# Kernel tuning notes

Measured on AMD Instinct MI355X. Metric: run time of the kernel, lower is better.

## Reference

```python
import jax, jax.numpy as jnp
import numpy as np

B, S, Dm = 2, 4096, 1024
H, HD = 8, 128            # num_heads, head_dim
WIN, STRIDE = 512, 256    # window_size, window_size // 2
NGT = 64                  # num_global_tokens


def setup_inputs() -> dict:
    key = jax.random.key(0)
    ks = jax.random.split(key, 6)
    sc = lambda k, shape: jax.random.normal(k, shape, jnp.float32) * 0.02
    return {
        "hidden_states": jax.random.normal(ks[0], (B, S, Dm), jnp.float32),
        "global_memory": jax.random.normal(ks[1], (1, H, NGT, HD), jnp.float32),
        "conv_w": sc(ks[2], (Dm, Dm, 4)),   # (out_ch, in_ch, kernel)
        "conv_b": jnp.zeros((Dm,), jnp.float32),
        "mix_w": sc(ks[3], (2 * Dm, Dm)),
        "mix_b": jnp.zeros((Dm,), jnp.float32),
        "out_w": sc(ks[4], (Dm, Dm)),
        "out_b": jnp.zeros((Dm,), jnp.float32),
    }


def _sliding_window(x):
    nw = (S - WIN) // STRIDE + 1
    idx = np.arange(nw)[:, None] * STRIDE + np.arange(WIN)[None, :]
    w = x[:, idx, :].reshape(B, nw, WIN, H, HD)
    att = jnp.einsum('bnqhd,bnkhd->bnhqk', w, w) / np.sqrt(HD).astype(np.float32)
    att = jax.nn.softmax(att, axis=-1)
    o = jnp.einsum('bnhqk,bnkhd->bnqhd', att, w).reshape(B, nw, WIN, Dm)
    # triangular-weighted overlap-add (every window has full length here)
    tri = jnp.linspace(0.5, 1.5, WIN, dtype=x.dtype)
    contrib = (o * tri[None, None, :, None]).reshape(B, nw * WIN, Dm)
    ids = jnp.asarray(idx.reshape(-1))
    num = jax.ops.segment_sum(jnp.moveaxis(contrib, 1, 0), ids, num_segments=S)  # (S,B,Dm)
    den = jax.ops.segment_sum(jnp.tile(tri, nw), ids, num_segments=S)            # (S,)
    return jnp.moveaxis(num, 0, 1) / jnp.maximum(den, 1e-6)[None, :, None]


def _compressed_global(x, gmem, cw, cb):
    # Conv1d(k=4, stride=4) == blockwise contraction over non-overlapping groups of 4
    comp = jnp.einsum('btkd,odk->bto', x.reshape(B, S // 4, 4, Dm), cw) + cb
    comp = comp[:, :NGT].reshape(B, NGT, H, HD).transpose(0, 2, 1, 3)  # (B,H,NGT,HD)
    kv = jnp.concatenate([comp, jnp.broadcast_to(gmem, (B, H, NGT, HD))], axis=2)
    q = x.reshape(B, S, H, HD).transpose(0, 2, 1, 3)                    # (B,H,S,HD)
    att = jax.nn.softmax(jnp.einsum('bhsd,bhtd->bhst', q, kv) / np.sqrt(HD).astype(np.float32), axis=-1)
    out = jnp.einsum('bhst,bhtd->bhsd', att, kv)
    return out.transpose(0, 2, 1, 3).reshape(B, S, Dm)


def _broadcast(x):
    # exponential diffusion: O(log n) roll steps (12 for S=4096)
    result = jnp.zeros_like(x)
    cur = x
    stride = 1
    while stride < S:
        cur = cur + 0.5 * (jnp.roll(cur, stride, axis=1) + jnp.roll(cur, -stride, axis=1))
        result = result + cur
        stride *= 2
    return result / np.float32(np.log2(S) + 1.0)


def reference(hidden_states, global_memory, conv_w, conv_b, mix_w, mix_b, out_w, out_b):
    local = _sliding_window(hidden_states)
    glob = _compressed_global(hidden_states, global_memory, conv_w, conv_b)
    bc = _broadcast(hidden_states)
    gate = jax.nn.sigmoid(jnp.concatenate([local, glob], axis=-1) @ mix_w + mix_b)
    mixed = gate * local + (1.0 - gate) * glob + bc
    return mixed @ out_w + out_b
```

## Files before the change

### kernel.cpp

```cpp
#include <hip/hip_runtime.h>
#include <cstdint>

#define B_   2
#define S_   4096
#define DM   1024
#define NH   8
#define HDIM 128
#define NWIN 15

typedef __attribute__((ext_vector_type(8))) short s8v;
typedef __attribute__((ext_vector_type(4))) float f4v;

__device__ __forceinline__ float f_lo(unsigned int u){
  union { unsigned int i; float f; } v; v.i = u << 16; return v.f;
}
__device__ __forceinline__ float f_hi(unsigned int u){
  union { unsigned int i; float f; } v; v.i = u & 0xffff0000u; return v.f;
}
__device__ __forceinline__ unsigned short f2bf(float f){
  unsigned int x = __float_as_uint(f);
  x += 0x7fffu + ((x >> 16) & 1u);
  return (unsigned short)(x >> 16);
}
__device__ __forceinline__ unsigned int pack2(float a, float b){
  return (unsigned int)f2bf(a) | ((unsigned int)f2bf(b) << 16);
}

__global__ __launch_bounds__(256) void k_cvtbf(const float* __restrict__ src,
                                               unsigned short* __restrict__ dst){
  size_t i = ((size_t)blockIdx.x*256 + threadIdx.x)*8;
  float4 a = *(const float4*)(src + i);
  float4 b = *(const float4*)(src + i + 4);
  uint4 r; r.x = pack2(a.x,a.y); r.y = pack2(a.z,a.w);
  r.z = pack2(b.x,b.y); r.w = pack2(b.z,b.w);
  *(uint4*)(dst + i) = r;
}

__global__ __launch_bounds__(256) void k_xposef(const float* __restrict__ x,
                                                float* __restrict__ xT){
  __shared__ float Ls[64][68];
  const int bid = blockIdx.x;
  const int b = bid>>10, r = bid&1023, st = r>>4, dt = r&15;
  const int s0 = st*64, d0 = dt*64;
  const int tid = threadIdx.x;
#pragma unroll
  for(int p=0;p<4;p++){
    int rr = p*16 + (tid>>4), c4 = (tid&15)*4;
    *(float4*)&Ls[rr][c4] = *(const float4*)(x + ((size_t)(b*S_)+s0+rr)*DM + d0 + c4);
  }
  __syncthreads();
#pragma unroll
  for(int p=0;p<4;p++){
    int dr = p*16 + (tid>>4), c4 = (tid&15)*4;
    float4 v = { Ls[c4+0][dr], Ls[c4+1][dr], Ls[c4+2][dr], Ls[c4+3][dr] };
    *(float4*)(xT + ((size_t)(b*DM)+d0+dr)*S_ + s0 + c4) = v;
  }
}

__global__ __launch_bounds__(256) void k_diffuseT(const float* __restrict__ xT,
                                                  unsigned short* __restrict__ bcT){
  __shared__ float bufA[2][4096];
  __shared__ float bufB[2][4096];
  const int b  = blockIdx.x >> 9;
  const int d0 = (blockIdx.x & 511) * 2;
  const int tid = threadIdx.x;
  float cur[32], res[32];
#pragma unroll
  for(int k=0;k<32;k++){
    int e = tid + (k<<8); int ch = e>>12; int s = e&4095;
    float v = xT[((size_t)(b*DM)+d0+ch)*S_ + s];
    cur[k] = v; res[k] = 0.f; bufA[ch][s] = v;
  }
  __syncthreads();
#pragma unroll 1
  for(int st=0; st<12; st++){
    const int stride = 1<<st;
    float (*src)[4096] = (st&1) ? bufB : bufA;
    float (*dst)[4096] = (st&1) ? bufA : bufB;
#pragma unroll
    for(int k=0;k<32;k++){
      int e = tid + (k<<8); int ch=e>>12; int s=e&4095;
      float c = cur[k] + 0.5f*(src[ch][(s-stride)&4095] + src[ch][(s+stride)&4095]);
      dst[ch][s] = c; cur[k] = c; res[k] += c;
    }
    __syncthreads();
  }
#pragma unroll
  for(int k=0;k<32;k++){
    int e = tid + (k<<8); int ch=e>>12; int s=e&4095;
    bcT[((size_t)(b*DM)+d0+ch)*S_ + s] = f2bf(res[k]*(1.0f/13.0f));
  }
}

__global__ __launch_bounds__(256) void k_bcxpose(const unsigned short* __restrict__ bcT,
                                                 unsigned short* __restrict__ bc){
  __shared__ unsigned short Ls[64*72];
  const int bid = blockIdx.x;
  const int b = bid>>10, r = bid&1023, st = r>>4, dt = r&15;
  const int s0 = st*64, d0 = dt*64;
  const int tid = threadIdx.x;
#pragma unroll
  for(int t=0;t<2;t++){
    int cl = tid + t*256; int dr = cl>>3, c = cl&7;
    *(uint4*)&Ls[dr*72 + c*8] = *(const uint4*)(bcT + ((size_t)(b*DM)+d0+dr)*S_ + s0 + c*8);
  }
  __syncthreads();
#pragma unroll
  for(int t=0;t<2;t++){
    int cl = tid + t*256; int sr = cl>>3, c = cl&7;
    unsigned short tmp[8];
#pragma unroll
    for(int j=0;j<8;j++) tmp[j] = Ls[(c*8+j)*72 + sr];
    *(uint4*)(bc + ((size_t)(b*S_)+s0+sr)*DM + d0 + c*8) = *(const uint4*)tmp;
  }
}

__global__ __launch_bounds__(256) void k_xstage(const float* __restrict__ x,
                                                unsigned short* __restrict__ Asta){
  __shared__ float xs[4][1024];
  const int m = blockIdx.x;
  const int b = m>>6, t = m&63;
  const int tid = threadIdx.x;
  const float* xp = x + (size_t)(b*S_ + 4*t)*DM;
  for(int i=tid; i<4096; i+=256) xs[i>>10][i&1023] = xp[i];
  __syncthreads();
  float v[16];
#pragma unroll
  for(int e=0; e<16; e++) v[e] = xs[e&3][tid*4 + (e>>2)];
  uint4 r0, r1;
  r0.x = pack2(v[0],v[1]);  r0.y = pack2(v[2],v[3]);
  r0.z = pack2(v[4],v[5]);  r0.w = pack2(v[6],v[7]);
  r1.x = pack2(v[8],v[9]);  r1.y = pack2(v[10],v[11]);
  r1.z = pack2(v[12],v[13]); r1.w = pack2(v[14],v[15]);
  unsigned short* op = Asta + (size_t)m*4096 + tid*16;
  *(uint4*)op = r0;
  *(uint4*)(op+8) = r1;
}

__global__ __launch_bounds__(256) void k_gemmconv(const unsigned short* __restrict__ A,
                                                  const unsigned short* __restrict__ Bw,
                                                  float* __restrict__ part){
  __shared__ __align__(16) unsigned short As[128*64];
  __shared__ __align__(16) unsigned short Bs[128*64];
  const int nt = blockIdx.x, kt = blockIdx.y;
  const int n0 = nt<<7;
  const int tid = threadIdx.x, wid = tid>>6, lane = tid&63, quad = lane>>4, tl = lane&15;
  const int mq = (wid&1)*64, nq = (wid>>1)*64;
  f4v acc[4][4];
#pragma unroll
  for(int i=0;i<4;i++)
#pragma unroll
    for(int j=0;j<4;j++) acc[i][j] = (f4v)(0.f);

  for(int kc=kt*1024; kc<kt*1024+1024; kc+=64){
    __syncthreads();
#pragma unroll
    for(int t=0; t<4; t++){
      int cl = tid + t*256, m = cl>>3, c = cl&7;
      uint4 v = *(const uint4*)(A + (size_t)m*4096 + kc + c*8);
      *(uint4*)&As[m*64 + ((c ^ (m&7))<<3)] = v;
      uint4 w = *(const uint4*)(Bw + (size_t)(n0+m)*4096 + kc + c*8);
      *(uint4*)&Bs[m*64 + ((c ^ (m&7))<<3)] = w;
    }
    __syncthreads();
#pragma unroll
    for(int ks=0; ks<2; ks++){
      s8v af[4], bf[4];
#pragma unroll
      for(int i=0;i<4;i++){
        int ml = mq + i*16 + tl;
        af[i] = *(const s8v*)&As[ml*64 + (((ks*4+quad) ^ (ml&7))<<3)];
      }
#pragma unroll
      for(int j=0;j<4;j++){
        int nl = nq + j*16 + tl;
        bf[j] = *(const s8v*)&Bs[nl*64 + (((ks*4+quad) ^ (nl&7))<<3)];
      }
#pragma unroll
      for(int i=0;i<4;i++)
#pragma unroll
        for(int j=0;j<4;j++)
          acc[i][j] = __builtin_amdgcn_mfma_f32_16x16x32_bf16(af[i], bf[j], acc[i][j], 0, 0, 0);
    }
  }
  float* pp = part + (size_t)kt*131072;
#pragma unroll
  for(int i=0;i<4;i++)
#pragma unroll
    for(int r=0;r<4;r++){
      int m = mq + i*16 + quad*4 + r;
#pragma unroll
      for(int j=0;j<4;j++){
        int n = n0 + nq + j*16 + tl;
        pp[m*1024 + n] = acc[i][j][r];
      }
    }
}

__global__ __launch_bounds__(256) void k_convred(const float* __restrict__ part,
                                                 const float* __restrict__ cb,
                                                 unsigned short* __restrict__ kv){
  int i = blockIdx.x*256 + threadIdx.x;
  int m = i>>10, o = i&1023;
  float v = part[i] + part[131072+i] + part[262144+i] + part[393216+i] + cb[o];
  int b = m>>6, t = m&63, h = o>>7, hd = o&127;
  kv[((size_t)(b*NH + h)*128 + t)*HDIM + hd] = f2bf(v);
}

__global__ __launch_bounds__(256) void k_gmem(const float* __restrict__ g,
                                              unsigned short* __restrict__ kv){
  int i = blockIdx.x*256 + threadIdx.x;
  int hd = i & 127, gt = (i>>7)&63, h = (i>>13)&7, b = i>>16;
  kv[((size_t)(b*NH + h)*128 + 64 + gt)*HDIM + hd] = f2bf(g[((size_t)(h*64 + gt))*HDIM + hd]);
}

template<int MODE>
__global__ __launch_bounds__(256) void k_attn(const unsigned short* __restrict__ xb,
                                              const unsigned short* __restrict__ kvb,
                                              unsigned short* __restrict__ outb){
  __shared__ __align__(16) unsigned short sh[26624];
  constexpr int KSo = 0;
  constexpr int VTo = 8192;
  constexpr int PSo = 17408;

  const int b = blockIdx.y;
  int h, n, qt, nkt;
  if(MODE==0){ int r = blockIdx.x; n = r>>5; h = (r>>2)&7; qt = r&3; nkt = 8; }
  else       { int r = blockIdx.x; h = r>>5; qt = r&31; n = 0; nkt = 2; }

  const int tid  = threadIdx.x;
  const int wid  = tid>>6, lane = tid&63, quad = lane>>4, tl = lane&15;
  const int sQ   = (MODE==0) ? (n*256 + qt*128) : (qt*128);

  s8v qf[2][4];
#pragma unroll
  for(int qi=0; qi<2; qi++){
    int qr = sQ + wid*32 + qi*16 + tl;
    const unsigned short* qp = xb + ((size_t)(b*S_) + qr)*DM + h*HDIM;
#pragma unroll
    for(int ks=0; ks<4; ks++)
      qf[qi][ks] = *(const s8v*)(qp + ks*32 + quad*8);
  }

  f4v oacc[8][2];
#pragma unroll
  for(int ht=0; ht<8; ht++){ oacc[ht][0] = (f4v)(0.f); oacc[ht][1] = (f4v)(0.f); }
  float m_[2] = {-1e30f, -1e30f}, l_[2] = {0.f, 0.f};

  for(int kt=0; kt<nkt; kt++){
    __syncthreads();
    const unsigned short* kp = (MODE==0)
        ? xb + ((size_t)(b*S_) + n*256 + kt*64)*DM + h*HDIM
        : kvb + ((size_t)(b*NH+h)*128 + kt*64)*HDIM;
    const int kstride = (MODE==0) ? DM : HDIM;
#pragma unroll
    for(int t=0; t<4; t++){
      int cl = tid + t*256, m = cl>>4, c = cl&15;
      uint4 v = *(const uint4*)(kp + (size_t)m*kstride + c*8);
      *(uint4*)&sh[KSo + m*128 + ((c ^ (m&7))<<3)] = v;
    }
    {
      int hd = tid&127, th = tid>>7;
#pragma unroll
      for(int tt=0; tt<8; tt++){
        int t0 = th*32 + tt*4;
        ushort4 u = { kp[(size_t)(t0+0)*kstride + hd], kp[(size_t)(t0+1)*kstride + hd],
                      kp[(size_t)(t0+2)*kstride + hd], kp[(size_t)(t0+3)*kstride + hd] };
        *(ushort4*)&sh[VTo + hd*72 + t0] = u;
      }
    }
    __syncthreads();

    f4v st[4][2];
#pragma unroll
    for(int tt=0; tt<4; tt++){
      st[tt][0] = (f4v)(0.f); st[tt][1] = (f4v)(0.f);
      int row = tt*16 + tl;
#pragma unroll
      for(int ks=0; ks<4; ks++){
        s8v af = *(const s8v*)&sh[KSo + row*128 + (((ks*4+quad) ^ (row&7))<<3)];
        st[tt][0] = __builtin_amdgcn_mfma_f32_16x16x32_bf16(af, qf[0][ks], st[tt][0], 0, 0, 0);
        st[tt][1] = __builtin_amdgcn_mfma_f32_16x16x32_bf16(af, qf[1][ks], st[tt][1], 0, 0, 0);
      }
    }

    const float SC = 0.08838834764831845f;
#pragma unroll
    for(int qi=0; qi<2; qi++){
      float mx = -1e30f;
#pragma unroll
      for(int tt=0; tt<4; tt++)
#pragma unroll
        for(int r=0; r<4; r++){
          float v = st[tt][qi][r]*SC;
          st[tt][qi][r] = v;
          mx = fmaxf(mx, v);
        }
      mx = fmaxf(mx, __shfl_xor(mx, 16));
      mx = fmaxf(mx, __shfl_xor(mx, 32));
      float nm = fmaxf(m_[qi], mx);
      float al = __expf(m_[qi] - nm);
      float ps = 0.f;
#pragma unroll
      for(int tt=0; tt<4; tt++)
#pragma unroll
        for(int r=0; r<4; r++){
          float p = __expf(st[tt][qi][r] - nm);
          st[tt][qi][r] = p; ps += p;
        }
      ps += __shfl_xor(ps, 16);
      ps += __shfl_xor(ps, 32);
      l_[qi] = l_[qi]*al + ps; m_[qi] = nm;
#pragma unroll
      for(int ht=0; ht<8; ht++) oacc[ht][qi] *= al;
      int ql = wid*32 + qi*16 + tl;
#pragma unroll
      for(int tt=0; tt<4; tt++){
        ushort4 u = { f2bf(st[tt][qi][0]), f2bf(st[tt][qi][1]),
                      f2bf(st[tt][qi][2]), f2bf(st[tt][qi][3]) };
        *(ushort4*)&sh[PSo + ql*72 + tt*16 + quad*4] = u;
      }
    }

#pragma unroll
    for(int kk=0; kk<2; kk++){
      s8v pb0 = *(const s8v*)&sh[PSo + (wid*32 + 0*16 + tl)*72 + kk*32 + quad*8];
      s8v pb1 = *(const s8v*)&sh[PSo + (wid*32 + 1*16 + tl)*72 + kk*32 + quad*8];
#pragma unroll
      for(int ht=0; ht<8; ht++){
        s8v vf = *(const s8v*)&sh[VTo + (ht*16 + tl)*72 + kk*32 + quad*8];
        oacc[ht][0] = __builtin_amdgcn_mfma_f32_16x16x32_bf16(vf, pb0, oacc[ht][0], 0, 0, 0);
        oacc[ht][1] = __builtin_amdgcn_mfma_f32_16x16x32_bf16(vf, pb1, oacc[ht][1], 0, 0, 0);
      }
    }
  }

#pragma unroll
  for(int qi=0; qi<2; qi++){
    float inv = 1.0f/l_[qi];
#pragma unroll
    for(int ht=0; ht<8; ht++) oacc[ht][qi] *= inv;
  }
  __syncthreads();
#pragma unroll
  for(int qi=0; qi<2; qi++){
    int ql = wid*32 + qi*16 + tl;
#pragma unroll
    for(int ht=0; ht<8; ht++){
      ushort4 u = { f2bf(oacc[ht][qi][0]), f2bf(oacc[ht][qi][1]),
                    f2bf(oacc[ht][qi][2]), f2bf(oacc[ht][qi][3]) };
      *(ushort4*)&sh[ql*136 + ht*16 + quad*4] = u;
    }
  }
  __syncthreads();
  {
    int ql = tid>>1, half = tid&1;
    size_t row = (MODE==0) ? (size_t)((b*NWIN + n)*512 + qt*128 + ql)
                           : (size_t)(b*S_ + qt*128 + ql);
    unsigned short* op = outb + row*DM + h*HDIM + half*64;
#pragma unroll
    for(int c=0; c<8; c++){
      uint4 v = *(const uint4*)&sh[ql*136 + half*64 + c*8];
      *(uint4*)(op + c*8) = v;
    }
  }
}

__global__ __launch_bounds__(256) void k_combine(const unsigned short* __restrict__ wso,
                                                 unsigned short* __restrict__ loc){
  const int bid = blockIdx.x;
  const int b = bid >> 12, s = bid & 4095;
  const int tid = threadIdx.x;
  const int nhi = s >> 8, sl = s & 255;
  const int c0 = tid*4;
  float n0=0.f, n1=0.f, n2=0.f, n3=0.f, den=0.f;
  if(nhi <= 14){
    float tr = 0.5f + (float)sl*(1.0f/511.0f);
    den += tr;
    uint2 u = *(const uint2*)(wso + (size_t)((b*NWIN + nhi)*512 + sl)*DM + c0);
    n0 += tr*f_lo(u.x); n1 += tr*f_hi(u.x); n2 += tr*f_lo(u.y); n3 += tr*f_hi(u.y);
  }
  if(nhi >= 1){
    int q2 = sl + 256;
    float tr = 0.5f + (float)q2*(1.0f/511.0f);
    den += tr;
    uint2 u = *(const uint2*)(wso + (size_t)((b*NWIN + nhi-1)*512 + q2)*DM + c0);
    n0 += tr*f_lo(u.x); n1 += tr*f_hi(u.x); n2 += tr*f_lo(u.y); n3 += tr*f_hi(u.y);
  }
  float di = 1.0f/den;
  uint2 o; o.x = pack2(n0*di, n1*di); o.y = pack2(n2*di, n3*di);
  *(uint2*)(loc + (size_t)(b*S_ + s)*DM + c0) = o;
}

__global__ __launch_bounds__(256) void k_wcvt(const float* __restrict__ W,
                                              unsigned short* __restrict__ WT, int K){
  __shared__ float Ls[64][68];
  int kt = blockIdx.x >> 4, nt = blockIdx.x & 15;
  int k0 = kt<<6, n0 = nt<<6;
  int tid = threadIdx.x;
#pragma unroll
  for(int p=0; p<4; p++){
    int r = p*16 + (tid>>4), c4 = (tid&15)*4;
    float4 v = *(const float4*)(W + (size_t)(k0+r)*1024 + n0 + c4);
    *(float4*)&Ls[r][c4] = v;
  }
  __syncthreads();
  int nn = tid>>2, kq = tid&3;
#pragma unroll
  for(int c=0; c<4; c++){
    int k = kq*16 + c*4;
    ushort4 u = { f2bf(Ls[k+0][nn]), f2bf(Ls[k+1][nn]), f2bf(Ls[k+2][nn]), f2bf(Ls[k+3][nn]) };
    *(ushort4*)(WT + (size_t)(n0+nn)*K + k0 + k) = u;
  }
}

template<int MODE>
__global__ __launch_bounds__(256) void k_gemm2(const unsigned short* __restrict__ A0,
                                               const unsigned short* __restrict__ A1,
                                               const unsigned short* __restrict__ WT,
                                               const float* __restrict__ bias,
                                               const unsigned short* __restrict__ loc,
                                               const unsigned short* __restrict__ glo,
                                               const unsigned short* __restrict__ bcb,
                                               unsigned short* __restrict__ outb,
                                               float* __restrict__ outf){
  const int KTOT = (MODE==0) ? 2048 : 1024;
  __shared__ __align__(16) unsigned short As[128*64];
  __shared__ __align__(16) unsigned short Bs[128*64];
  const int mt = blockIdx.x >> 3, nt = blockIdx.x & 7;
  const int m0 = mt<<7, n0 = nt<<7;
  const int tid = threadIdx.x, wid = tid>>6, lane = tid&63, quad = lane>>4, tl = lane&15;
  const int mq = (wid&1)*64, nq = (wid>>1)*64;
  f4v acc[4][4];
#pragma unroll
  for(int i=0;i<4;i++)
#pragma unroll
    for(int j=0;j<4;j++) acc[i][j] = (f4v)(0.f);

  for(int kc=0; kc<KTOT; kc+=64){
    __syncthreads();
    const unsigned short* Ab = (MODE==0 && kc>=1024) ? A1 : A0;
    const int kb = (MODE==0) ? (kc & 1023) : kc;
#pragma unroll
    for(int t=0; t<4; t++){
      int cl = tid + t*256, m = cl>>3, c = cl&7;
      uint4 v = *(const uint4*)(Ab + (size_t)(m0+m)*1024 + kb + c*8);
      *(uint4*)&As[m*64 + ((c ^ (m&7))<<3)] = v;
      uint4 w = *(const uint4*)(WT + (size_t)(n0+m)*KTOT + kc + c*8);
      *(uint4*)&Bs[m*64 + ((c ^ (m&7))<<3)] = w;
    }
    __syncthreads();
#pragma unroll
    for(int ks=0; ks<2; ks++){
      s8v af[4], bf[4];
#pragma unroll
      for(int i=0;i<4;i++){
        int ml = mq + i*16 + tl;
        af[i] = *(const s8v*)&As[ml*64 + (((ks*4+quad) ^ (ml&7))<<3)];
      }
#pragma unroll
      for(int j=0;j<4;j++){
        int nl = nq + j*16 + tl;
        bf[j] = *(const s8v*)&Bs[nl*64 + (((ks*4+quad) ^ (nl&7))<<3)];
      }
#pragma unroll
      for(int i=0;i<4;i++)
#pragma unroll
        for(int j=0;j<4;j++)
          acc[i][j] = __builtin_amdgcn_mfma_f32_16x16x32_bf16(af[i], bf[j], acc[i][j], 0, 0, 0);
    }
  }

#pragma unroll
  for(int i=0;i<4;i++){
#pragma unroll
    for(int r=0;r<4;r++){
      int m = m0 + mq + i*16 + quad*4 + r;
      size_t rowb = (size_t)m * 1024;
#pragma unroll
      for(int j=0;j<4;j++){
        int nn = n0 + nq + j*16 + tl;
        float v = acc[i][j][r] + bias[nn];
        if(MODE==0){
          float g  = 1.0f/(1.0f + __expf(-v));
          float lv = f_lo((unsigned int)loc[rowb+nn]);
          float gv = f_lo((unsigned int)glo[rowb+nn]);
          float bv = f_lo((unsigned int)bcb[rowb+nn]);
          outb[rowb+nn] = f2bf(g*lv + (1.0f-g)*gv + bv);
        } else {
          outf[rowb+nn] = v;
        }
      }
    }
  }
}

extern "C" void kernel_launch(void* const* d_in, const int* in_sizes, int n_in,
                              void* d_out, int out_size, void* d_ws, size_t ws_size,
                              hipStream_t stream){
  const float* x  = (const float*)d_in[0];
  const float* gm = (const float*)d_in[1];
  const float* cw = (const float*)d_in[2];
  const float* cb = (const float*)d_in[3];
  const float* mw = (const float*)d_in[4];
  const float* mb = (const float*)d_in[5];
  const float* ow = (const float*)d_in[6];
  const float* ob = (const float*)d_in[7];
  float* out = (float*)d_out;

  char* ws = (char*)d_ws;
  const size_t SZ = (size_t)B_*S_*DM*2;
  unsigned short* localb = (unsigned short*)(ws);
  unsigned short* globb  = (unsigned short*)(ws + SZ);
  unsigned short* bcb    = (unsigned short*)(ws + 2*SZ);
  unsigned short* kvb    = (unsigned short*)(ws + 3*SZ);
  unsigned short* wso    = (unsigned short*)(ws + 3*SZ + 524288);
  unsigned short* mixed  = wso;
  unsigned short* wt1    = (unsigned short*)(ws + 3*SZ + 524288 + SZ);
  unsigned short* wt2    = (unsigned short*)(ws + 3*SZ + 524288 + SZ + 4194304);
  unsigned short* cwb    = (unsigned short*)(ws);
  unsigned short* asta   = (unsigned short*)(ws + 8388608);
  float*          cpart  = (float*)        (ws + 9437184);
  float*          xT     = (float*)(ws + SZ);
  unsigned short* bcT    = wso;
  unsigned short* xbf    = (unsigned short*)(ws);

  k_cvtbf   <<<2048, 256, 0, stream>>>(cw, cwb);
  k_xstage  <<<128,  256, 0, stream>>>(x, asta);
  k_gemmconv<<<dim3(8,4), 256, 0, stream>>>(asta, cwb, cpart);
  k_convred <<<512,  256, 0, stream>>>(cpart, cb, kvb);
  k_gmem    <<<512,  256, 0, stream>>>(gm, kvb);
  k_xposef  <<<2048, 256, 0, stream>>>(x, xT);
  k_diffuseT<<<1024, 256, 0, stream>>>(xT, bcT);
  k_bcxpose <<<2048, 256, 0, stream>>>(bcT, bcb);
  k_cvtbf   <<<4096, 256, 0, stream>>>(x, xbf);
  k_attn<1> <<<dim3(256,2), 256, 0, stream>>>(xbf, kvb, globb);
  k_attn<0> <<<dim3(480,2), 256, 0, stream>>>(xbf, kvb, wso);
  k_combine <<<8192, 256, 0, stream>>>(wso, localb);
  k_wcvt    <<<512,  256, 0, stream>>>(mw, wt1, 2048);
  k_wcvt    <<<256,  256, 0, stream>>>(ow, wt2, 1024);
  k_gemm2<0><<<512, 256, 0, stream>>>(localb, globb, wt1, mb, localb, globb, bcb, mixed, nullptr);
  k_gemm2<1><<<512, 256, 0, stream>>>(mixed, nullptr, wt2, ob, nullptr, nullptr, nullptr, nullptr, out);
}
```

Baseline: 437.8 us.

## Prefetch K/V tiles into registers, lazy softmax rescale, swizzle P buffer

The attention kernel now loads the next K/V tile into registers during compute and builds the transposed V tile in shared memory from register shuffles instead of strided scalar global loads. Softmax works in exp2 with a folded scale and rescales the running max only when any lane's max exceeds it by a threshold. The P tile uses an XOR-swizzled layout with a smaller stride, shrinking shared memory, and launch bounds request 3 blocks per CU. This hides global latency and removes uncoalesced loads, at the cost of more registers and a small deviation from exact online softmax.

After: 416.2 us. -4.9%, faster.

```diff
diff --git a/kernel.cpp b/kernel.cpp
--- a/kernel.cpp
+++ b/kernel.cpp
@@ -215,10 +215,10 @@
 }
 
 template<int MODE>
-__global__ __launch_bounds__(256) void k_attn(const unsigned short* __restrict__ xb,
-                                              const unsigned short* __restrict__ kvb,
-                                              unsigned short* __restrict__ outb){
-  __shared__ __align__(16) unsigned short sh[26624];
+__global__ __launch_bounds__(256, 3) void k_attn(const unsigned short* __restrict__ xb,
+                                                 const unsigned short* __restrict__ kvb,
+                                                 unsigned short* __restrict__ outb){
+  __shared__ __align__(16) unsigned short sh[25600];
   constexpr int KSo = 0;
   constexpr int VTo = 8192;
   constexpr int PSo = 17408;
@@ -242,34 +242,55 @@
       qf[qi][ks] = *(const s8v*)(qp + ks*32 + quad*8);
   }
 
+  const unsigned short* kbase = (MODE==0)
+      ? xb + ((size_t)(b*S_) + n*256)*DM + h*HDIM
+      : kvb + (size_t)(b*NH+h)*128*HDIM;
+  const int kstride = (MODE==0) ? DM : HDIM;
+  const int mrow = (tid&15)*4;
+  const int cg   = tid>>4;
+
+  uint4 rg[4];
+#pragma unroll
+  for(int j=0;j<4;j++)
+    rg[j] = *(const uint4*)(kbase + (size_t)(mrow+j)*kstride + cg*8);
+
   f4v oacc[8][2];
 #pragma unroll
   for(int ht=0; ht<8; ht++){ oacc[ht][0] = (f4v)(0.f); oacc[ht][1] = (f4v)(0.f); }
   float m_[2] = {-1e30f, -1e30f}, l_[2] = {0.f, 0.f};
 
+  const float SC2 = 0.12751743f;
+
   for(int kt=0; kt<nkt; kt++){
     __syncthreads();
-    const unsigned short* kp = (MODE==0)
-        ? xb + ((size_t)(b*S_) + n*256 + kt*64)*DM + h*HDIM
-        : kvb + ((size_t)(b*NH+h)*128 + kt*64)*HDIM;
-    const int kstride = (MODE==0) ? DM : HDIM;
-#pragma unroll
-    for(int t=0; t<4; t++){
-      int cl = tid + t*256, m = cl>>4, c = cl&15;
-      uint4 v = *(const uint4*)(kp + (size_t)m*kstride + c*8);
-      *(uint4*)&sh[KSo + m*128 + ((c ^ (m&7))<<3)] = v;
+#pragma unroll
+    for(int j=0;j<4;j++){
+      int t = mrow + j;
+      *(uint4*)&sh[KSo + t*128 + ((cg ^ (t&7))<<3)] = rg[j];
     }
     {
-      int hd = tid&127, th = tid>>7;
-#pragma unroll
-      for(int tt=0; tt<8; tt++){
-        int t0 = th*32 + tt*4;
-        ushort4 u = { kp[(size_t)(t0+0)*kstride + hd], kp[(size_t)(t0+1)*kstride + hd],
-                      kp[(size_t)(t0+2)*kstride + hd], kp[(size_t)(t0+3)*kstride + hd] };
-        *(ushort4*)&sh[VTo + hd*72 + t0] = u;
-      }
-    }
-    __syncthreads();
+      const unsigned int* w0 = (const unsigned int*)&rg[0];
+      const unsigned int* w1 = (const unsigned int*)&rg[1];
+      const unsigned int* w2 = (const unsigned int*)&rg[2];
+      const unsigned int* w3 = (const unsigned int*)&rg[3];
+#pragma unroll
+      for(int i=0;i<8;i++){
+        int w = i>>1;
+        unsigned int a, c2;
+        if(i&1){ a  = (w0[w]>>16) | (w1[w] & 0xffff0000u);
+                 c2 = (w2[w]>>16) | (w3[w] & 0xffff0000u); }
+        else   { a  = (w0[w] & 0xffffu) | (w1[w]<<16);
+                 c2 = (w2[w] & 0xffffu) | (w3[w]<<16); }
+        uint2 u = {a, c2};
+        *(uint2*)&sh[VTo + (cg*8+i)*72 + mrow] = u;
+      }
+    }
+    __syncthreads();
+    if(kt+1 < nkt){
+      const unsigned short* np = kbase + (size_t)((kt+1)*64 + mrow)*kstride + cg*8;
+#pragma unroll
+      for(int j=0;j<4;j++) rg[j] = *(const uint4*)(np + (size_t)j*kstride);
+    }
 
     f4v st[4][2];
 #pragma unroll
@@ -284,48 +305,48 @@
       }
     }
 
-    const float SC = 0.08838834764831845f;
 #pragma unroll
     for(int qi=0; qi<2; qi++){
-      float mx = -1e30f;
-#pragma unroll
-      for(int tt=0; tt<4; tt++)
-#pragma unroll
-        for(int r=0; r<4; r++){
-          float v = st[tt][qi][r]*SC;
-          st[tt][qi][r] = v;
-          mx = fmaxf(mx, v);
-        }
+      float ma = fmaxf(fmaxf(st[0][qi][0],st[0][qi][1]), fmaxf(st[0][qi][2],st[0][qi][3]));
+      float mb = fmaxf(fmaxf(st[1][qi][0],st[1][qi][1]), fmaxf(st[1][qi][2],st[1][qi][3]));
+      float mc = fmaxf(fmaxf(st[2][qi][0],st[2][qi][1]), fmaxf(st[2][qi][2],st[2][qi][3]));
+      float md = fmaxf(fmaxf(st[3][qi][0],st[3][qi][1]), fmaxf(st[3][qi][2],st[3][qi][3]));
+      float mx = fmaxf(fmaxf(ma,mb), fmaxf(mc,md));
       mx = fmaxf(mx, __shfl_xor(mx, 16));
       mx = fmaxf(mx, __shfl_xor(mx, 32));
-      float nm = fmaxf(m_[qi], mx);
-      float al = __expf(m_[qi] - nm);
+      if(!__all(mx <= m_[qi] + 60.0f)){
+        float al = exp2f((m_[qi] - mx)*SC2);
+        l_[qi] *= al;
+#pragma unroll
+        for(int ht=0; ht<8; ht++) oacc[ht][qi] *= al;
+        m_[qi] = mx;
+      }
+      float mm = m_[qi];
       float ps = 0.f;
 #pragma unroll
       for(int tt=0; tt<4; tt++)
 #pragma unroll
         for(int r=0; r<4; r++){
-          float p = __expf(st[tt][qi][r] - nm);
+          float p = exp2f((st[tt][qi][r] - mm)*SC2);
           st[tt][qi][r] = p; ps += p;
         }
       ps += __shfl_xor(ps, 16);
       ps += __shfl_xor(ps, 32);
-      l_[qi] = l_[qi]*al + ps; m_[qi] = nm;
-#pragma unroll
-      for(int ht=0; ht<8; ht++) oacc[ht][qi] *= al;
+      l_[qi] += ps;
       int ql = wid*32 + qi*16 + tl;
 #pragma unroll
       for(int tt=0; tt<4; tt++){
         ushort4 u = { f2bf(st[tt][qi][0]), f2bf(st[tt][qi][1]),
                       f2bf(st[tt][qi][2]), f2bf(st[tt][qi][3]) };
-        *(ushort4*)&sh[PSo + ql*72 + tt*16 + quad*4] = u;
+        *(ushort4*)&sh[PSo + ql*64 + (((tt*2 + (quad>>1)) ^ (ql&7))<<3) + (quad&1)*4] = u;
       }
     }
 
 #pragma unroll
     for(int kk=0; kk<2; kk++){
-      s8v pb0 = *(const s8v*)&sh[PSo + (wid*32 + 0*16 + tl)*72 + kk*32 + quad*8];
-      s8v pb1 = *(const s8v*)&sh[PSo + (wid*32 + 1*16 + tl)*72 + kk*32 + quad*8];
+      int ql0 = wid*32 + tl, ql1 = wid*32 + 16 + tl;
+      s8v pb0 = *(const s8v*)&sh[PSo + ql0*64 + (((kk*4+quad) ^ (ql0&7))<<3)];
+      s8v pb1 = *(const s8v*)&sh[PSo + ql1*64 + (((kk*4+quad) ^ (ql1&7))<<3)];
 #pragma unroll
       for(int ht=0; ht<8; ht++){
         s8v vf = *(const s8v*)&sh[VTo + (ht*16 + tl)*72 + kk*32 + quad*8];
```
